# Kernel tuning notes

Hardware: AMD Instinct MI355X
Metric: run time of the kernel (lower is better)

## Reference

```python
import jax, jax.numpy as jnp
import numpy as np

N, E = 50000, 800000
IN_DIM, H, D = 128, 8, 16  # num_heads=8, out_dim(per head)=16


def setup_inputs() -> dict:
    key = jax.random.key(0)
    ks = jax.random.split(key, 9)
    s = 1.0 / np.sqrt(IN_DIM)
    return {
        "h": jax.random.normal(ks[0], (N, IN_DIM), dtype=jnp.float32),
        "Wq": jax.random.normal(ks[1], (IN_DIM, H * D), dtype=jnp.float32) * s,
        "bq": jnp.zeros((H * D,), dtype=jnp.float32),
        "Wk": jax.random.normal(ks[2], (IN_DIM, H * D), dtype=jnp.float32) * s,
        "bk": jnp.zeros((H * D,), dtype=jnp.float32),
        "Wv": jax.random.normal(ks[3], (IN_DIM, H * D), dtype=jnp.float32) * s,
        "bv": jnp.zeros((H * D,), dtype=jnp.float32),
        "src": jax.random.randint(ks[4], (E,), 0, N, dtype=jnp.int32),
        "dst": jax.random.randint(ks[5], (E,), 0, N, dtype=jnp.int32),
    }


def reference(h, Wq, bq, Wk, bk, Wv, bv, src, dst):
    n = h.shape[0]
    Q = (h @ Wq + bq).reshape(n, H, D)
    K = (h @ Wk + bk).reshape(n, H, D)
    V = (h @ Wv + bv).reshape(n, H, D)
    # edge score: u_mul_v(K, Q).sum(-1) / sqrt(D), clamped to [-5, 5]
    score = jnp.einsum("ehd,ehd->eh", K[src], Q[dst]) / jnp.sqrt(
        jnp.asarray(D, h.dtype)
    )  # [E, H]
    score = jnp.clip(score, -5.0, 5.0)
    # edge_softmax over edges sharing the same destination node
    smax = jax.ops.segment_max(score, dst, num_segments=n)  # [N, H]
    ex = jnp.exp(score - smax[dst])
    denom = jax.ops.segment_sum(ex, dst, num_segments=n)  # [N, H]
    a = ex / denom[dst]  # [E, H]
    # u_mul_e(V, a) then sum to destination
    m = V[src] * a[:, :, None]  # [E, H, D]
    wV = jax.ops.segment_sum(m, dst, num_segments=n)  # [N, H, D]
    return wV.reshape(n, H * D)
```

## Files before the change

kernel.cpp:

```cpp
#include <hip/hip_runtime.h>
#include <hip/hip_bf16.h>


typedef short short8 __attribute__((ext_vector_type(8)));
typedef float f32x4 __attribute__((ext_vector_type(4)));

__device__ __forceinline__ unsigned pack_bf16(float a, float b) {
    unsigned ua = __float_as_uint(a), ub = __float_as_uint(b);
    ua += 0x7fffu + ((ua >> 16) & 1u);
    ub += 0x7fffu + ((ub >> 16) & 1u);
    return (ua >> 16) | (ub & 0xffff0000u);
}

#define ULO(u) __uint_as_float((u) << 16)
#define UHI(u) __uint_as_float((u) & 0xffff0000u)

__global__ __launch_bounds__(256) void prep_all(
    const float* __restrict__ W0, const float* __restrict__ W1,
    const float* __restrict__ W2, unsigned char* __restrict__ WTb,
    int* __restrict__ counts, int n)
{
    const int b = blockIdx.x;
    if (b < 24) {
        const int w   = b >> 3;
        const int idx = (b & 7) * 256 + threadIdx.x;
        const float* W = (w == 0) ? W0 : (w == 1) ? W1 : W2;
        unsigned char* wt = WTb + w * 32768;
        const int kp = idx >> 5;
        const int c4 = (idx & 31) * 4;
        const float* Wp = W + (size_t)(2 * kp) * 128 + c4;
        float4 wa = *(const float4*)Wp;
        float4 wb = *(const float4*)(Wp + 128);
        float a0[4] = {wa.x, wa.y, wa.z, wa.w};
        float a1[4] = {wb.x, wb.y, wb.z, wb.w};
#pragma unroll
        for (int i = 0; i < 4; ++i) {
            const int col = c4 + i;
            *(unsigned*)(wt + col * 256 + ((4 * kp) ^ ((col & 7) << 4))) =
                pack_bf16(a0[i], a1[i]);
        }
    } else {
        const int i = (b - 24) * 256 + threadIdx.x;
        if (i < n) counts[i] = 0;
    }
}

__global__ void hist_rank(const int* __restrict__ dst, int* __restrict__ counts,
                          int* __restrict__ rank, int e) {
    int i = blockIdx.x * blockDim.x + threadIdx.x;
    if (i < e) rank[i] = atomicAdd(&counts[dst[i]], 1);
}

__global__ void scan_block_sums(const int* __restrict__ counts, int* __restrict__ bsums, int nelem) {
    __shared__ int red[4];
    int i = blockIdx.x * 256 + threadIdx.x;
    int v = (i < nelem) ? counts[i] : 0;
#pragma unroll
    for (int o = 32; o > 0; o >>= 1) v += __shfl_down(v, o, 64);
    if ((threadIdx.x & 63) == 0) red[threadIdx.x >> 6] = v;
    __syncthreads();
    if (threadIdx.x == 0) bsums[blockIdx.x] = red[0] + red[1] + red[2] + red[3];
}

__global__ void scan_final2(const int* __restrict__ counts, const int* __restrict__ bsums,
                            int* __restrict__ offsets, int nelem, int e) {
    __shared__ int tmp[256];
    __shared__ int red[4];
    const int t = threadIdx.x;

    int pre = (t < blockIdx.x) ? bsums[t] : 0;
#pragma unroll
    for (int o = 32; o > 0; o >>= 1) pre += __shfl_down(pre, o, 64);
    if ((t & 63) == 0) red[t >> 6] = pre;
    __syncthreads();
    const int base = red[0] + red[1] + red[2] + red[3];

    const int i = blockIdx.x * 256 + t;
    int v = (i < nelem) ? counts[i] : 0;
    tmp[t] = v;
    __syncthreads();
    for (int o = 1; o < 256; o <<= 1) {
        int u = (t >= o) ? tmp[t - o] : 0;
        __syncthreads();
        tmp[t] += u;
        __syncthreads();
    }
    if (i < nelem) offsets[i] = base + tmp[t] - v;
    if (i == nelem) offsets[nelem] = e;
}

__global__ void fill_kernel(const int* __restrict__ src, const int* __restrict__ dst,
                            const int* __restrict__ rank, const int* __restrict__ offsets,
                            int* __restrict__ srcSorted, int e) {
    int i = blockIdx.x * blockDim.x + threadIdx.x;
    if (i < e) srcSorted[offsets[dst[i]] + rank[i]] = src[i];
}

__global__ __launch_bounds__(512) void qkv_gemm(
    const float* __restrict__ h, const unsigned char* __restrict__ WTb,
    const float* __restrict__ b0, const float* __restrict__ b1,
    const float* __restrict__ b2,
    unsigned* __restrict__ qb, unsigned* __restrict__ kb, unsigned* __restrict__ vb,
    int n)
{
    __shared__ __align__(16) unsigned char lds[32768];
    const int tid  = threadIdx.x;
    const int row0 = blockIdx.x * 64;

    for (int idx = tid; idx < 2048; idx += 512) {
        const int row = idx >> 5;
        const int c4  = (idx & 31) * 4;
        float4 v = make_float4(0.f, 0.f, 0.f, 0.f);
        if (row0 + row < n) v = *(const float4*)(h + (size_t)(row0 + row) * 128 + c4);
        *(uint2*)(lds + row * 256 + ((c4 * 2) ^ ((row & 7) << 4))) =
            make_uint2(pack_bf16(v.x, v.y), pack_bf16(v.z, v.w));
    }

    const float* bs[3] = {b0, b1, b2};
    unsigned* planes[3] = {qb, kb, vb};

    const int lane = tid & 63, wave = tid >> 6;
    const int wr = wave >> 2, wc = wave & 3;
    const int lr = lane & 15, lg = lane >> 4;

    __syncthreads();

    short8 af[2][4];
#pragma unroll
    for (int mt = 0; mt < 2; ++mt)
#pragma unroll
        for (int ks = 0; ks < 4; ++ks) {
            const int row = wr * 32 + mt * 16 + lr;
            const int kbyte = ks * 64 + lg * 16;
            af[mt][ks] = *(const short8*)(lds + row * 256 + (kbyte ^ ((row & 7) << 4)));
        }

    for (int w = 0; w < 3; ++w) {
        short8 bf[2][4];
#pragma unroll
        for (int nt = 0; nt < 2; ++nt)
#pragma unroll
            for (int ks = 0; ks < 4; ++ks) {
                const int col = wc * 32 + nt * 16 + lr;
                const int kbyte = ks * 64 + lg * 16;
                bf[nt][ks] = *(const short8*)(
                    WTb + w * 32768 + col * 256 + (kbyte ^ ((col & 7) << 4)));
            }

        f32x4 acc[2][2];
#pragma unroll
        for (int nt = 0; nt < 2; ++nt) {
            const float bv = bs[w][wc * 32 + nt * 16 + lr];
            acc[0][nt] = (f32x4){bv, bv, bv, bv};
            acc[1][nt] = (f32x4){bv, bv, bv, bv};
        }
#pragma unroll
        for (int ks = 0; ks < 4; ++ks)
#pragma unroll
            for (int mt = 0; mt < 2; ++mt)
#pragma unroll
                for (int nt = 0; nt < 2; ++nt)
                    acc[mt][nt] = __builtin_amdgcn_mfma_f32_16x16x32_bf16(
                        af[mt][ks], bf[nt][ks], acc[mt][nt], 0, 0, 0);

        __syncthreads();
        {
            unsigned* epi = (unsigned*)(lds + 16384);
#pragma unroll
            for (int mt = 0; mt < 2; ++mt)
#pragma unroll
                for (int nt = 0; nt < 2; ++nt) {
                    const int col = wc * 32 + nt * 16 + lr;
#pragma unroll
                    for (int r = 0; r < 4; ++r) {
                        const int row = wr * 32 + mt * 16 + lg * 4 + r;
                        const float v  = acc[mt][nt][r];
                        const float vn = __shfl_xor(v, 1);
                        if (!(lane & 1)) epi[row * 64 + (col >> 1)] = pack_bf16(v, vn);
                    }
                }
        }
        __syncthreads();
        {
            const uint4* s = (const uint4*)(lds + 16384);
            uint4* d = (uint4*)(planes[w] + (size_t)row0 * 64);
            d[tid]       = s[tid];
            d[tid + 512] = s[tid + 512];
        }
    }
}

__global__ __launch_bounds__(256) void mha_node(
    const unsigned* __restrict__ Qb, const unsigned* __restrict__ Kb,
    const unsigned* __restrict__ Vb,
    const int* __restrict__ offsets, const int* __restrict__ srcSorted,
    float* __restrict__ out, int n)
{
    const int lane = threadIdx.x & 63;
    const int node = (blockIdx.x * blockDim.x + threadIdx.x) >> 6;
    if (node >= n) return;

    const float QS = 0.25f * 1.44269504089f;
    const float CL = 5.f * 1.44269504089f;

    const unsigned qu = Qb[(size_t)node * 64 + lane];
    const float qx = ULO(qu) * QS, qy = UHI(qu) * QS;
    const int beg = offsets[node], end = offsets[node + 1];

    float accx = 0.f, accy = 0.f, lsum = 0.f;

#define EDGE_COMPUTE(ku, vu)                                          \
    {                                                                 \
        float prod = fmaf(ULO(ku), qx, UHI(ku) * qy);                 \
        prod += __shfl_xor(prod, 1);                                  \
        prod += __shfl_xor(prod, 2);                                  \
        prod += __shfl_xor(prod, 4);                                  \
        float sc = fminf(CL, fmaxf(-CL, prod));                       \
        float p = exp2f(sc);                                          \
        lsum += p;                                                    \
        accx = fmaf(p, ULO(vu), accx);                                \
        accy = fmaf(p, UHI(vu), accy);                                \
    }

    for (int j0 = beg; j0 < end; j0 += 64) {
        const int rem = end - j0;
        const int cnt = rem < 64 ? rem : 64;
        int myS = (lane < cnt) ? srcSorted[j0 + lane] : 0;

        int t = 0;
        for (; t + 8 <= cnt; t += 8) {
            unsigned ku[8], vu[8];
#pragma unroll
            for (int u = 0; u < 8; ++u) {
                int s = __shfl(myS, t + u);
                ku[u] = Kb[(size_t)s * 64 + lane];
                vu[u] = Vb[(size_t)s * 64 + lane];
            }
#pragma unroll
            for (int u = 0; u < 8; ++u) EDGE_COMPUTE(ku[u], vu[u]);
        }
        for (; t < cnt; ++t) {
            int s = __shfl(myS, t);
            unsigned ku0 = Kb[(size_t)s * 64 + lane];
            unsigned vu0 = Vb[(size_t)s * 64 + lane];
            EDGE_COMPUTE(ku0, vu0);
        }
    }

    float inv = (lsum > 0.f) ? 1.f / lsum : 0.f;
    *(float2*)(out + (size_t)node * 128 + lane * 2) =
        make_float2(accx * inv, accy * inv);
}

extern "C" void kernel_launch(void* const* d_in, const int* in_sizes, int n_in,
                              void* d_out, int out_size, void* d_ws, size_t ws_size,
                              hipStream_t stream) {
    const float* h  = (const float*)d_in[0];
    const float* Wq = (const float*)d_in[1];
    const float* bq = (const float*)d_in[2];
    const float* Wk = (const float*)d_in[3];
    const float* bk = (const float*)d_in[4];
    const float* Wv = (const float*)d_in[5];
    const float* bv = (const float*)d_in[6];
    const int*   src = (const int*)d_in[7];
    const int*   dst = (const int*)d_in[8];
    float* out = (float*)d_out;

    const int n = in_sizes[0] / 128;
    const int e = in_sizes[7];
    const int nblk = (n + 63) / 64;
    const int npad = nblk * 64;
    const int nb = (n + 255) / 256;

    char* ws = (char*)d_ws;
    size_t off = 0;
    auto alloc = [&](size_t bytes) {
        char* p = ws + off;
        off = (off + bytes + 255) & ~(size_t)255;
        return p;
    };
    unsigned char* WTb = (unsigned char*)alloc(3 * 32768);
    unsigned* Qb       = (unsigned*)alloc((size_t)npad * 64 * 4);
    unsigned* Kb       = (unsigned*)alloc((size_t)npad * 64 * 4);
    unsigned* Vb       = (unsigned*)alloc((size_t)npad * 64 * 4);
    int* counts        = (int*)alloc((size_t)n * sizeof(int));
    int* offsets       = (int*)alloc((size_t)(n + 1) * sizeof(int));
    int* rank          = (int*)alloc((size_t)e * sizeof(int));
    int* bsums         = (int*)alloc((size_t)nb * sizeof(int));
    int* srcSorted     = (int*)alloc((size_t)e * sizeof(int));
    (void)ws_size; (void)n_in; (void)out_size;

    prep_all<<<24 + nb, 256, 0, stream>>>(Wq, Wk, Wv, WTb, counts, n);
    hist_rank<<<(e + 255) / 256, 256, 0, stream>>>(dst, counts, rank, e);
    scan_block_sums<<<nb, 256, 0, stream>>>(counts, bsums, n);
    scan_final2<<<nb, 256, 0, stream>>>(counts, bsums, offsets, n, e);
    fill_kernel<<<(e + 255) / 256, 256, 0, stream>>>(src, dst, rank, offsets, srcSorted, e);
    qkv_gemm<<<nblk, 512, 0, stream>>>(h, WTb, bq, bk, bv, Qb, Kb, Vb, n);
    mha_node<<<((size_t)n * 64 + 255) / 256, 256, 0, stream>>>(
        Qb, Kb, Vb, offsets, srcSorted, out, n);
}
```

Before: 145.0 us.

## Process two edges per wavefront with half-wave split and 8-byte loads

Each wavefront now splits into two 32-lane halves. Each half handles a different edge, loading 8 bytes of K and V per lane, so each lane covers 4 features instead of 2. This halves the loop iterations and the dot-product shuffle reductions per edge, and uses wider gathers. In exchange it needs a cross-half reduction at the end, and the tail loop masks out the invalid half, leaving some work idle.

```diff
diff --git a/kernel.cpp b/kernel.cpp
--- a/kernel.cpp
+++ b/kernel.cpp
@@ -191,35 +191,42 @@
 }
 
 __global__ __launch_bounds__(256) void mha_node(
-    const unsigned* __restrict__ Qb, const unsigned* __restrict__ Kb,
-    const unsigned* __restrict__ Vb,
+    const unsigned* __restrict__ Qb, const uint2* __restrict__ Kb2,
+    const uint2* __restrict__ Vb2,
     const int* __restrict__ offsets, const int* __restrict__ srcSorted,
     float* __restrict__ out, int n)
 {
     const int lane = threadIdx.x & 63;
     const int node = (blockIdx.x * blockDim.x + threadIdx.x) >> 6;
     if (node >= n) return;
+    const int half = lane >> 5;
+    const int l5   = lane & 31;
 
     const float QS = 0.25f * 1.44269504089f;
     const float CL = 5.f * 1.44269504089f;
 
-    const unsigned qu = Qb[(size_t)node * 64 + lane];
-    const float qx = ULO(qu) * QS, qy = UHI(qu) * QS;
+    const uint2 qu = *(const uint2*)(Qb + (size_t)node * 64 + 2 * l5);
+    const float q0 = ULO(qu.x) * QS, q1 = UHI(qu.x) * QS;
+    const float q2 = ULO(qu.y) * QS, q3 = UHI(qu.y) * QS;
+
     const int beg = offsets[node], end = offsets[node + 1];
-
-    float accx = 0.f, accy = 0.f, lsum = 0.f;
-
-#define EDGE_COMPUTE(ku, vu)                                          \
-    {                                                                 \
-        float prod = fmaf(ULO(ku), qx, UHI(ku) * qy);                 \
-        prod += __shfl_xor(prod, 1);                                  \
-        prod += __shfl_xor(prod, 2);                                  \
-        prod += __shfl_xor(prod, 4);                                  \
-        float sc = fminf(CL, fmaxf(-CL, prod));                       \
-        float p = exp2f(sc);                                          \
-        lsum += p;                                                    \
-        accx = fmaf(p, ULO(vu), accx);                                \
-        accy = fmaf(p, UHI(vu), accy);                                \
+    float a0 = 0.f, a1 = 0.f, a2 = 0.f, a3 = 0.f, lsum = 0.f;
+
+#define PAIR_COMPUTE(ku, vu, val)                                       \
+    {                                                                   \
+        float prod = ULO((ku).x) * q0;                                  \
+        prod = fmaf(UHI((ku).x), q1, prod);                             \
+        prod = fmaf(ULO((ku).y), q2, prod);                             \
+        prod = fmaf(UHI((ku).y), q3, prod);                             \
+        prod += __shfl_xor(prod, 1);                                    \
+        prod += __shfl_xor(prod, 2);                                    \
+        float sc = fminf(CL, fmaxf(-CL, prod));                         \
+        float p = (val) ? exp2f(sc) : 0.f;                              \
+        lsum += p;                                                      \
+        a0 = fmaf(p, ULO((vu).x), a0);                                  \
+        a1 = fmaf(p, UHI((vu).x), a1);                                  \
+        a2 = fmaf(p, ULO((vu).y), a2);                                  \
+        a3 = fmaf(p, UHI((vu).y), a3);                                  \
     }
 
     for (int j0 = beg; j0 < end; j0 += 64) {
@@ -229,27 +236,37 @@
 
         int t = 0;
         for (; t + 8 <= cnt; t += 8) {
-            unsigned ku[8], vu[8];
-#pragma unroll
-            for (int u = 0; u < 8; ++u) {
-                int s = __shfl(myS, t + u);
-                ku[u] = Kb[(size_t)s * 64 + lane];
-                vu[u] = Vb[(size_t)s * 64 + lane];
+            uint2 ku[4], vu[4];
+#pragma unroll
+            for (int u = 0; u < 4; ++u) {
+                int s = __shfl(myS, t + 2 * u + half);
+                ku[u] = Kb2[(size_t)s * 32 + l5];
+                vu[u] = Vb2[(size_t)s * 32 + l5];
             }
 #pragma unroll
-            for (int u = 0; u < 8; ++u) EDGE_COMPUTE(ku[u], vu[u]);
-        }
-        for (; t < cnt; ++t) {
-            int s = __shfl(myS, t);
-            unsigned ku0 = Kb[(size_t)s * 64 + lane];
-            unsigned vu0 = Vb[(size_t)s * 64 + lane];
-            EDGE_COMPUTE(ku0, vu0);
-        }
-    }
-
-    float inv = (lsum > 0.f) ? 1.f / lsum : 0.f;
-    *(float2*)(out + (size_t)node * 128 + lane * 2) =
-        make_float2(accx * inv, accy * inv);
+            for (int u = 0; u < 4; ++u) PAIR_COMPUTE(ku[u], vu[u], true);
+        }
+        for (; t < cnt; t += 2) {
+            const int ei = t + half;
+            const bool val = ei < cnt;
+            int s = __shfl(myS, val ? ei : cnt - 1);
+            uint2 ku0 = Kb2[(size_t)s * 32 + l5];
+            uint2 vu0 = Vb2[(size_t)s * 32 + l5];
+            PAIR_COMPUTE(ku0, vu0, val);
+        }
+    }
+
+    lsum += __shfl_xor(lsum, 32);
+    a0 += __shfl_xor(a0, 32);
+    a1 += __shfl_xor(a1, 32);
+    a2 += __shfl_xor(a2, 32);
+    a3 += __shfl_xor(a3, 32);
+
+    if (half == 0) {
+        const float inv = (lsum > 0.f) ? 1.f / lsum : 0.f;
+        *(float4*)(out + (size_t)node * 128 + 4 * l5) =
+            make_float4(a0 * inv, a1 * inv, a2 * inv, a3 * inv);
+    }
 }
 
 extern "C" void kernel_launch(void* const* d_in, const int* in_sizes, int n_in,
@@ -297,5 +314,5 @@
     fill_kernel<<<(e + 255) / 256, 256, 0, stream>>>(src, dst, rank, offsets, srcSorted, e);
     qkv_gemm<<<nblk, 512, 0, stream>>>(h, WTb, bq, bk, bv, Qb, Kb, Vb, n);
     mha_node<<<((size_t)n * 64 + 255) / 256, 256, 0, stream>>>(
-        Qb, Kb, Vb, offsets, srcSorted, out, n);
-}
+        Qb, (const uint2*)Kb, (const uint2*)Vb, offsets, srcSorted, out, n);
+}
```

Result: no change. 142.2 us, median of 2 (-1.9%).
